# Kernel optimization log

Hardware: AMD Instinct MI355X
Metric: run time of the kernel (lower is better)

Reference implementation:

```python
import jax, jax.numpy as jnp
import numpy as np

N_TX, N_ACC, N_MER = 100000, 50000, 5000
HID, HEADS, OUT_CH, LAYERS = 128, 4, 64, 3
HC = HID * HEADS  # 512, concat-heads width
SRC_T = ['tx', 'tx', 'tx', 'acc', 'acc', 'mer']
DST_T = ['acc', 'acc', 'mer', 'tx', 'tx', 'tx']


def setup_inputs():
    key = jax.random.key(0)
    ks = jax.random.split(key, 16)
    rn = lambda k, s: jax.random.normal(k, s, dtype=jnp.float32) * 0.05
    n_of = {'tx': N_TX, 'acc': N_ACC, 'mer': N_MER}
    E = N_TX  # one sender-acct / receiver-acct / merchant edge per transaction
    src = jnp.stack([jax.random.randint(jax.random.fold_in(ks[0], r), (E,), 0, n_of[SRC_T[r]]) for r in range(6)])
    dst = jnp.stack([jax.random.randint(jax.random.fold_in(ks[1], r), (E,), 0, n_of[DST_T[r]]) for r in range(6)])
    edges = jnp.stack([src, dst], axis=1).astype(jnp.int32)  # [6, 2, E] (rel, src/dst, edge)
    return dict(
        x_tx=rn(ks[2], (N_TX, 64)), x_acc=rn(ks[3], (N_ACC, 32)), x_mer=rn(ks[4], (N_MER, 32)),
        Wtx=rn(ks[5], (64, HID)), btx=jnp.zeros((HID,), jnp.float32),
        Wacc=rn(ks[6], (32, HID)), bacc=jnp.zeros((HID,), jnp.float32),
        Wmer=rn(ks[7], (32, HID)), bmer=jnp.zeros((HID,), jnp.float32),
        W0=rn(ks[8], (6, HID, HC)),            # layer-0 GAT linear per relation
        Wrest=rn(ks[9], (LAYERS - 1, 6, HC, HC)),  # layers 1..L-1
        att_s=rn(ks[10], (LAYERS, 6, HEADS, HID)),
        att_d=rn(ks[11], (LAYERS, 6, HEADS, HID)),
        att_b=jnp.zeros((LAYERS, 6, HC), jnp.float32),
        bn_g=jnp.ones((LAYERS, HC), jnp.float32), bn_b=jnp.zeros((LAYERS, HC), jnp.float32),
        Wh1=rn(ks[12], (HC, OUT_CH)), bh1=jnp.zeros((OUT_CH,), jnp.float32),
        Wh2=rn(ks[13], (OUT_CH, 1)), bh2=jnp.zeros((1,), jnp.float32),
        edges=edges)


def _gat_rel(x_src, x_dst, src, dst, W, a_s, a_d, b, n_dst):
    """PyG GATConv (shared lin, add_self_loops=False, concat heads), eval mode."""
    H, C = a_s.shape
    hs = (x_src @ W).reshape(-1, H, C)  # [Ns, H, C]
    hd = (x_dst @ W).reshape(-1, H, C)  # [Nd, H, C]
    e = jax.nn.leaky_relu((hs * a_s).sum(-1)[src] + (hd * a_d).sum(-1)[dst], 0.2)  # [E, H]
    m = jax.lax.stop_gradient(jax.ops.segment_max(e, dst, num_segments=n_dst))
    ex = jnp.exp(e - m[dst])
    denom = jax.ops.segment_sum(ex, dst, num_segments=n_dst)
    alpha = ex / (denom[dst] + 1e-16)  # segment softmax over in-edges of each dst
    out = jax.ops.segment_sum(alpha[:, :, None] * hs[src], dst, num_segments=n_dst)
    return out.reshape(n_dst, H * C) + b


def _forward(x_tx, x_acc, x_mer, Wtx, btx, Wacc, bacc, Wmer, bmer, W0, Wrest,
             att_s, att_d, att_b, bn_g, bn_b, Wh1, bh1, Wh2, bh2, edges):
    h = {'tx': jax.nn.relu(x_tx @ Wtx + btx),
         'acc': jax.nn.relu(x_acc @ Wacc + bacc),
         'mer': jax.nn.relu(x_mer @ Wmer + bmer)}
    n_of = {'tx': x_tx.shape[0], 'acc': x_acc.shape[0], 'mer': x_mer.shape[0]}
    for i in range(LAYERS):
        Wl = W0 if i == 0 else Wrest[i - 1]
        new = {k: jnp.zeros((n_of[k], HC), x_tx.dtype) for k in n_of}  # HeteroConv aggr='sum'
        for r in range(6):
            o = _gat_rel(h[SRC_T[r]], h[DST_T[r]], edges[r, 0], edges[r, 1],
                         Wl[r], att_s[i, r], att_d[i, r], att_b[i, r], n_of[DST_T[r]])
            new[DST_T[r]] = new[DST_T[r]] + o
        t = new['tx']  # BatchNorm1d (batch statistics) on transaction nodes only
        mu = t.mean(0)
        var = t.var(0)
        new['tx'] = (t - mu) / jnp.sqrt(var + 1e-5) * bn_g[i] + bn_b[i]
        new = {k: jax.nn.relu(v) for k, v in new.items()}
        if i > 0:  # residual from second layer on
            new = {k: new[k] + h[k] for k in new}
        h = new
    hidden = jax.nn.relu(h['tx'] @ Wh1 + bh1)
    return (hidden @ Wh2 + bh2).squeeze(-1)  # [N_tx] logits


def reference(x_tx, x_acc, x_mer, Wtx, btx, Wacc, bacc, Wmer, bmer, W0, Wrest,
              att_s, att_d, att_b, bn_g, bn_b, Wh1, bh1, Wh2, bh2, edges):
    return _forward(x_tx, x_acc, x_mer, Wtx, btx, Wacc, bacc, Wmer, bmer, W0, Wrest,
                    att_s, att_d, att_b, bn_g, bn_b, Wh1, bh1, Wh2, bh2, edges)
```

## Files before the change

### kernel.cpp

```cpp
#include <hip/hip_runtime.h>
#include <math.h>


typedef unsigned short BF16;
typedef short short8 __attribute__((ext_vector_type(8)));
typedef float f32x4 __attribute__((ext_vector_type(4)));
typedef __bf16 bf16x8 __attribute__((ext_vector_type(8)));

static __device__ __forceinline__ float lrelu(float x){ return x > 0.f ? x : 0.2f*x; }

__device__ __forceinline__ float ldE(const float* p, long i){ return p[i]; }
__device__ __forceinline__ float ldE(const BF16* p, long i){
  return __uint_as_float((unsigned)p[i] << 16);
}
__device__ __forceinline__ void stE(float* p, long i, float v){ p[i] = v; }
__device__ __forceinline__ void stE(BF16* p, long i, float v){
  unsigned u = __float_as_uint(v);
  p[i] = (BF16)((u + 0x7FFFu + ((u >> 16) & 1u)) >> 16);
}
__device__ __forceinline__ BF16 f2bf(float v){
  unsigned u = __float_as_uint(v);
  return (BF16)((u + 0x7FFFu + ((u >> 16) & 1u)) >> 16);
}
__device__ __forceinline__ float bf2f(short s){
  return __uint_as_float((unsigned)(unsigned short)s << 16);
}
__device__ __forceinline__ float4 ld4E(const float* p, long i){ return *(const float4*)(p + i); }
__device__ __forceinline__ float4 ld4E(const BF16* p, long i){
  ushort4 s = *(const ushort4*)(p + i);
  return make_float4(__uint_as_float((unsigned)s.x<<16), __uint_as_float((unsigned)s.y<<16),
                     __uint_as_float((unsigned)s.z<<16), __uint_as_float((unsigned)s.w<<16));
}

__global__ void k_zero(int* __restrict__ p, long n){
  long i = (long)blockIdx.x*blockDim.x + threadIdx.x;
  if (i < n) p[i] = 0;
}
__global__ void k_fill_f32(float* __restrict__ p, long n, float v){
  long i = (long)blockIdx.x*blockDim.x + threadIdx.x;
  if (i < n) p[i] = v;
}

__global__ __launch_bounds__(256) void k_wt(const float* __restrict__ in, BF16* __restrict__ out,
                                            int K, int N)
{
  __shared__ float t[32][33];
  int kb = blockIdx.y*32, nb = blockIdx.x*32;
  int tx = threadIdx.x & 31, ty8 = threadIdx.x >> 5;
  for (int j = ty8; j < 32; j += 8){
    int k = kb + j, n = nb + tx;
    t[j][tx] = (k < K && n < N) ? in[(long)k*N + n] : 0.f;
  }
  __syncthreads();
  for (int j = ty8; j < 32; j += 8){
    int n = nb + j, k = kb + tx;
    if (n < N && k < K) out[(long)n*K + k] = f2bf(t[tx][j]);
  }
}

__global__ __launch_bounds__(256) void k_foldAll(
    const float* __restrict__ Wbase, long wstride,
    const float* __restrict__ atts, const float* __restrict__ attd,
    float* __restrict__ F, int Din)
{
  int w = (blockIdx.x*256 + threadIdx.x) >> 6;
  int lane = threadIdx.x & 63;
  int total = 48*Din;
  if (w >= total) return;
  int k = w % Din;
  int rem = w / Din;
  int h = rem & 3, sd = (rem >> 2) & 1, r = rem >> 3;
  const float* wr = Wbase + (long)r*wstride + (long)k*512 + h*128;
  const float* ar = (sd ? attd : atts) + r*512 + h*128;
  float p = wr[lane]*ar[lane] + wr[lane+64]*ar[lane+64];
  #pragma unroll
  for (int off = 32; off; off >>= 1) p += __shfl_down(p, off, 64);
  if (lane == 0) F[(long)((r*2+sd)*4 + h)*Din + k] = p;
}

template<int BN, int WM, int WN, int FM, int FN, typename TC>
__global__ __launch_bounds__(256) void k_mfma(
    const BF16* __restrict__ A, const BF16* __restrict__ Bt, TC* __restrict__ C,
    int M, int K, int c0, int ldc, const float* __restrict__ bias, int doRelu)
{
  constexpr int BM = 128;
  constexpr int LSTR = 72;
  __shared__ __attribute__((aligned(16))) short Als[BM][LSTR];
  __shared__ __attribute__((aligned(16))) short Bls[BN][LSTR];
  const int bn0 = blockIdx.x * BN;
  const int bm = blockIdx.y*BM;
  const int tid = threadIdx.x;
  const int wave = tid >> 6, lane = tid & 63;
  const int wr = wave / WN, wc = wave % WN;
  const int lrow = lane & 15, kg = lane >> 4;
  f32x4 acc[FM][FN] = {};
  for (int k0 = 0; k0 < K; k0 += 64){
    #pragma unroll
    for (int t = 0; t < 4; ++t){
      int idx = tid + t*256;
      int row = idx >> 3, kc = (idx & 7) << 3;
      int gr = bm + row;
      short8 v = {};
      if (gr < M) v = *(const short8*)(A + (long)gr*K + k0 + kc);
      *(short8*)&Als[row][kc] = v;
    }
    #pragma unroll
    for (int t = 0; t < BN/32; ++t){
      int idx = tid + t*256;
      int row = idx >> 3, kc = (idx & 7) << 3;
      *(short8*)&Bls[row][kc] = *(const short8*)(Bt + (long)(c0+bn0+row)*K + k0 + kc);
    }
    __syncthreads();
    #pragma unroll
    for (int kk = 0; kk < 2; ++kk){
      short8 af[FM], bq[FN];
      #pragma unroll
      for (int m = 0; m < FM; ++m)
        af[m] = *(const short8*)&Als[wr*FM*16 + m*16 + lrow][kk*32 + kg*8];
      #pragma unroll
      for (int n = 0; n < FN; ++n)
        bq[n] = *(const short8*)&Bls[wc*FN*16 + n*16 + lrow][kk*32 + kg*8];
      #pragma unroll
      for (int m = 0; m < FM; ++m)
        #pragma unroll
        for (int n = 0; n < FN; ++n)
          acc[m][n] = __builtin_amdgcn_mfma_f32_16x16x32_bf16(
              __builtin_bit_cast(bf16x8, af[m]), __builtin_bit_cast(bf16x8, bq[n]),
              acc[m][n], 0, 0, 0);
    }
    __syncthreads();
  }
  #pragma unroll
  for (int m = 0; m < FM; ++m){
    #pragma unroll
    for (int n = 0; n < FN; ++n){
      #pragma unroll
      for (int j = 0; j < 4; ++j){
        int row = bm + wr*FM*16 + m*16 + kg*4 + j;
        if (row >= M) continue;
        int col = wc*FN*16 + n*16 + lrow;
        float v = acc[m][n][j];
        if (bias) v += bias[bn0 + col];
        if (doRelu) v = fmaxf(v, 0.f);
        stE(C, (long)row*ldc + bn0 + col, v);
      }
    }
  }
}

template<typename TA, typename TC>
__global__ __launch_bounds__(256) void k_gemm(
    const TA* __restrict__ A, const float* __restrict__ B, TC* __restrict__ C,
    int M, int N, int K, int ldb, const float* __restrict__ bias, int doRelu)
{
  __shared__ float As[16][64];
  __shared__ float Bs[16][64];
  const int bm = blockIdx.y*64, bn = blockIdx.x*64;
  const int tid = threadIdx.x;
  const int ty = tid >> 4, tx = tid & 15;
  const int ar = tid >> 2;
  const int ac = (tid & 3) << 2;
  const int br = tid >> 4;
  const int bc = (tid & 15) << 2;
  float acc[4][4] = {};
  for (int k0 = 0; k0 < K; k0 += 16){
    int row = bm + ar;
    float4 av = make_float4(0.f,0.f,0.f,0.f);
    if (row < M) av = ld4E(A, (long)row*K + k0 + ac);
    As[ac+0][ar]=av.x; As[ac+1][ar]=av.y; As[ac+2][ar]=av.z; As[ac+3][ar]=av.w;
    float4 bv = make_float4(0.f,0.f,0.f,0.f);
    if (bn + bc + 3 < N) bv = *(const float4*)(B + (long)(k0+br)*ldb + bn + bc);
    *(float4*)&Bs[br][bc] = bv;
    __syncthreads();
    #pragma unroll
    for (int kk = 0; kk < 16; ++kk){
      float a[4], b[4];
      #pragma unroll
      for (int x = 0; x < 4; ++x){ a[x]=As[kk][ty*4+x]; b[x]=Bs[kk][tx*4+x]; }
      #pragma unroll
      for (int y = 0; y < 4; ++y)
        #pragma unroll
        for (int x = 0; x < 4; ++x) acc[y][x] += a[y]*b[x];
    }
    __syncthreads();
  }
  #pragma unroll
  for (int y = 0; y < 4; ++y){
    int row = bm + ty*4 + y;
    if (row >= M) continue;
    #pragma unroll
    for (int x = 0; x < 4; ++x){
      int col = bn + tx*4 + x;
      if (col >= N) continue;
      float v = acc[y][x];
      if (bias) v += bias[col];
      if (doRelu) v = fmaxf(v, 0.f);
      stE(C, (long)row*N + col, v);
    }
  }
}

template<int R>
__global__ __launch_bounds__(256) void k_scoreM(
    const BF16* __restrict__ X, const float* __restrict__ Ftab, long fstride,
    float* __restrict__ out, long ostride, int N, int Din)
{
  int wave = threadIdx.x >> 6, lane = threadIdx.x & 63;
  int node0 = blockIdx.x*16 + wave*4;
  if (node0 >= N) return;
  int base = lane*8;
  bool act = base < Din;
  float x[4][8];
  #pragma unroll
  for (int t = 0; t < 4; ++t){
    int node = node0 + t;
    if (act && node < N){
      short8 v = *(const short8*)(X + (long)node*Din + base);
      #pragma unroll
      for (int j = 0; j < 8; ++j) x[t][j] = bf2f(v[j]);
    } else {
      #pragma unroll
      for (int j = 0; j < 8; ++j) x[t][j] = 0.f;
    }
  }
  #pragma unroll
  for (int r = 0; r < R; ++r){
    const float* F = Ftab + (long)r*fstride;
    float p[4][4] = {};
    #pragma unroll
    for (int h = 0; h < 4; ++h){
      float f[8];
      if (act){
        float4 fa = *(const float4*)(F + h*Din + base);
        float4 fb = *(const float4*)(F + h*Din + base + 4);
        f[0]=fa.x; f[1]=fa.y; f[2]=fa.z; f[3]=fa.w;
        f[4]=fb.x; f[5]=fb.y; f[6]=fb.z; f[7]=fb.w;
      } else {
        #pragma unroll
        for (int j = 0; j < 8; ++j) f[j] = 0.f;
      }
      #pragma unroll
      for (int t = 0; t < 4; ++t)
        #pragma unroll
        for (int j = 0; j < 8; ++j) p[t][h] += x[t][j]*f[j];
    }
    #pragma unroll
    for (int t = 0; t < 4; ++t)
      #pragma unroll
      for (int h = 0; h < 4; ++h)
        #pragma unroll
        for (int off = 32; off; off >>= 1)
          p[t][h] += __shfl_down(p[t][h], off, 64);
    if (lane == 0){
      #pragma unroll
      for (int t = 0; t < 4; ++t){
        int node = node0 + t;
        if (node < N){
          #pragma unroll
          for (int h = 0; h < 4; ++h)
            out[(long)r*ostride + (long)node*4 + h] = p[t][h];
        }
      }
    }
  }
}

__global__ void k_hist(const int* __restrict__ dst, int* __restrict__ counts, int E, int nd){
  int e = blockIdx.x*blockDim.x + threadIdx.x;
  if (e >= E) return;
  int d = dst[e];
  if ((unsigned)d < (unsigned)nd) atomicAdd(&counts[d], 1);
}
__global__ void k_scan1(const int* __restrict__ counts, int* __restrict__ indptr,
                        int* __restrict__ bsums, int n)
{
  __shared__ int sm[256];
  int i = blockIdx.x*256 + threadIdx.x;
  int v = (i < n) ? counts[i] : 0;
  sm[threadIdx.x] = v; __syncthreads();
  for (int off = 1; off < 256; off <<= 1){
    int t = (threadIdx.x >= off) ? sm[threadIdx.x - off] : 0;
    __syncthreads();
    sm[threadIdx.x] += t;
    __syncthreads();
  }
  if (i < n) indptr[i+1] = sm[threadIdx.x];
  if (threadIdx.x == 255) bsums[blockIdx.x] = sm[255];
  if (blockIdx.x == 0 && threadIdx.x == 0) indptr[0] = 0;
}
__global__ void k_scan2(int* __restrict__ bsums, int nb){
  __shared__ int sm[1024];
  int t = threadIdx.x;
  int v = (t < nb) ? bsums[t] : 0;
  sm[t] = v; __syncthreads();
  for (int off = 1; off < 1024; off <<= 1){
    int x = (t >= off) ? sm[t - off] : 0;
    __syncthreads();
    sm[t] += x;
    __syncthreads();
  }
  if (t < nb) bsums[t] = sm[t];
}
__global__ void k_scan3(int* __restrict__ indptr, const int* __restrict__ bsums, int n){
  if (blockIdx.x == 0) return;
  int i = blockIdx.x*256 + threadIdx.x;
  int add = bsums[blockIdx.x - 1];
  if (i < n) indptr[i+1] += add;
}
__global__ void k_scatter(const int* __restrict__ src, const int* __restrict__ dst,
                          const int* __restrict__ indptr, int* __restrict__ cursor,
                          int* __restrict__ esrc, int E, int nd, int ns)
{
  int e = blockIdx.x*blockDim.x + threadIdx.x;
  if (e >= E) return;
  int d = dst[e];
  if ((unsigned)d >= (unsigned)nd) return;
  int s = src[e];
  if ((unsigned)s >= (unsigned)ns) s = 0;
  int pos = indptr[d] + atomicAdd(&cursor[d], 1);
  if (pos >= 0 && pos < E) esrc[pos] = s;
}

__global__ __launch_bounds__(256) void k_alpha(
    const float* __restrict__ ss, const float* __restrict__ sd,
    const int* __restrict__ indptr, const int* __restrict__ esrc,
    float* __restrict__ alpha, int n_dst, int E, int ns)
{
  int wid = (blockIdx.x*blockDim.x + threadIdx.x) >> 6;
  int lane = threadIdx.x & 63;
  if (wid >= n_dst) return;
  int e0 = indptr[wid], e1 = indptr[wid+1];
  e0 = max(0, min(e0, E)); e1 = max(e0, min(e1, E));
  if (e0 >= e1) return;
  int h = lane >> 4, g = lane & 15;
  float sdl = sd[(long)wid*4 + h];
  float m = -INFINITY;
  for (int e = e0 + g; e < e1; e += 16){
    int s = esrc[e]; if ((unsigned)s >= (unsigned)ns) s = 0;
    m = fmaxf(m, lrelu(ss[(long)s*4 + h] + sdl));
  }
  #pragma unroll
  for (int o = 1; o < 16; o <<= 1) m = fmaxf(m, __shfl_xor(m, o, 16));
  float den = 0.f;
  for (int e = e0 + g; e < e1; e += 16){
    int s = esrc[e]; if ((unsigned)s >= (unsigned)ns) s = 0;
    den += __expf(lrelu(ss[(long)s*4 + h] + sdl) - m);
  }
  #pragma unroll
  for (int o = 1; o < 16; o <<= 1) den += __shfl_xor(den, o, 16);
  float inv = 1.f/(den + 1e-16f);
  for (int e = e0 + g; e < e1; e += 16){
    int s = esrc[e]; if ((unsigned)s >= (unsigned)ns) s = 0;
    alpha[(long)e*4 + h] = __expf(lrelu(ss[(long)s*4 + h] + sdl) - m) * inv;
  }
}

__device__ __forceinline__ void agg_body(
    const BF16* __restrict__ Zt, const float* __restrict__ alpha,
    const int* __restrict__ indptr, const int* __restrict__ esrc,
    float* acc, int NJ, int wid, int lane, int TW, int head0, int E, int ns)
{
  int e0 = indptr[wid], e1 = indptr[wid+1];
  e0 = max(0, min(e0, E)); e1 = max(e0, min(e1, E));
  for (int e = e0; e < e1; ++e){
    int s = esrc[e]; if ((unsigned)s >= (unsigned)ns) s = 0;
    float aA = alpha[(long)e*4 + head0];
    float aB = (NJ == 4) ? alpha[(long)e*4 + head0 + 1] : aA;
    const BF16* zr = Zt + (long)s*TW;
    #pragma unroll 4
    for (int j = 0; j < NJ; ++j){
      int col = lane + 64*j;
      if (col < TW) acc[j] += ((NJ == 4 && j >= 2) ? aB : aA) * ldE(zr, col);
    }
  }
}
template<int NJ>
__global__ __launch_bounds__(256) void k_agg(
    const BF16* __restrict__ Zt, const float* __restrict__ alpha,
    const int* __restrict__ indptr, const int* __restrict__ esrc,
    BF16* __restrict__ out, int ldc, int c0w, int TW, int head0,
    int accum, int n_dst, int E, int ns)
{
  int wid = (blockIdx.x*blockDim.x + threadIdx.x) >> 6;
  int lane = threadIdx.x & 63;
  if (wid >= n_dst) return;
  float acc[NJ];
  #pragma unroll
  for (int j = 0; j < NJ; ++j) acc[j] = 0.f;
  agg_body(Zt, alpha, indptr, esrc, acc, NJ, wid, lane, TW, head0, E, ns);
  #pragma unroll
  for (int j = 0; j < NJ; ++j){
    int col = lane + 64*j;
    if (col < TW){
      long idx = (long)wid*ldc + c0w + col;
      float v = acc[j];
      if (accum) v += ldE(out, idx);
      stE(out, idx, v);
    }
  }
}

template<int NJ>
__global__ __launch_bounds__(256) void k_agg3(
    const BF16* __restrict__ Z0, const BF16* __restrict__ Z1, const BF16* __restrict__ Z2,
    const float* __restrict__ a0, const float* __restrict__ a1, const float* __restrict__ a2,
    const int* __restrict__ ip0, const int* __restrict__ ip1, const int* __restrict__ ip2,
    const int* __restrict__ es0, const int* __restrict__ es1, const int* __restrict__ es2,
    BF16* __restrict__ out, int ldc, int TW, int head0,
    int n_dst, int E, int ns0, int ns1, int ns2)
{
  int wid = (blockIdx.x*blockDim.x + threadIdx.x) >> 6;
  int lane = threadIdx.x & 63;
  if (wid >= n_dst) return;
  float acc[NJ];
  #pragma unroll
  for (int j = 0; j < NJ; ++j) acc[j] = 0.f;
  agg_body(Z0, a0, ip0, es0, acc, NJ, wid, lane, TW, head0, E, ns0);
  agg_body(Z1, a1, ip1, es1, acc, NJ, wid, lane, TW, head0, E, ns1);
  agg_body(Z2, a2, ip2, es2, acc, NJ, wid, lane, TW, head0, E, ns2);
  #pragma unroll
  for (int j = 0; j < NJ; ++j){
    int col = lane + 64*j;
    if (col < TW) stE(out, (long)wid*ldc + col, acc[j]);
  }
}

__global__ void k_bnp(const BF16* __restrict__ nw, float* __restrict__ bnp,
                      int N, int TW, int P)
{
  int col  = threadIdx.x & (TW - 1);
  int slot = threadIdx.x / TW;
  int rpb  = 256 / TW;
  int p    = blockIdx.x*rpb + slot;
  float s = 0.f, s2 = 0.f;
  for (long r = p; r < N; r += P){
    float v = ldE(nw, r*TW + col);
    s += v; s2 += v*v;
  }
  bnp[(long)p*2*TW + col]      = s;
  bnp[(long)p*2*TW + TW + col] = s2;
}
__global__ void k_bnf(const float* __restrict__ bnp, float* __restrict__ bns,
                      int P, int TW)
{
  int c = blockIdx.x*256 + threadIdx.x;
  if (c >= 2*TW) return;
  float s = 0.f;
  for (int p = 0; p < P; ++p) s += bnp[(long)p*2*TW + c];
  bns[c] = s;
}
__global__ void k_bn_apply(const BF16* __restrict__ nw, const float* __restrict__ bns,
                           const float* __restrict__ g, const float* __restrict__ b,
                           BF16* __restrict__ A, int N, int TW, int c0, int res)
{
  long total = (long)N*TW;
  for (long i = (long)blockIdx.x*blockDim.x + threadIdx.x; i < total;
       i += (long)gridDim.x*blockDim.x){
    int col = (int)(i % TW);
    long r  = i / TW;
    float mu  = bns[col] / (float)N;
    float var = bns[TW + col] / (float)N - mu*mu;
    int gc = c0 + col;
    float sc = g[gc] * rsqrtf(var + 1e-5f);
    float sh = b[gc] - mu*sc;
    float v = fmaxf(ldE(nw, i)*sc + sh, 0.f);
    long ai = r*512 + gc;
    if (res) v += ldE(A, ai);
    stE(A, ai, v);
  }
}

__global__ void k_update(const BF16* __restrict__ B, const float* __restrict__ ab1,
                         const float* __restrict__ ab2, BF16* __restrict__ A,
                         long n512, int res)
{
  for (long i = (long)blockIdx.x*blockDim.x + threadIdx.x; i < n512;
       i += (long)gridDim.x*blockDim.x){
    int c = (int)(i & 511);
    float v = ldE(B, i) + ab1[c] + (ab2 ? ab2[c] : 0.f);
    v = fmaxf(v, 0.f);
    if (res) v += ldE(A, i);
    stE(A, i, v);
  }
}

__global__ void k_logits(const BF16* __restrict__ Hid, const float* __restrict__ Wh2,
                         const float* __restrict__ bh2, float* __restrict__ out, int N)
{
  int node = (blockIdx.x*blockDim.x + threadIdx.x) >> 6;
  int lane = threadIdx.x & 63;
  if (node >= N) return;
  float v = ldE(Hid, (long)node*64 + lane) * Wh2[lane];
  #pragma unroll
  for (int off = 32; off; off >>= 1) v += __shfl_down(v, off, 64);
  if (lane == 0) out[node] = v + bh2[0];
}

struct Arena {
  BF16 *A[3];
  BF16 *Bst[3];
  BF16 *Zt;
  BF16 *nwtile;
  BF16 *hidden;
  float *scoreS, *scoreD;
  float *alpha;
  float *Fbuf;
  float *bnp, *bns;
  int *counts, *bsums;
  int *indptr[6], *esrc[6];
  BF16 *Wt0[6], *WtL[2][6], *Wh1t;
  size_t total;
};

extern "C" void kernel_launch(void* const* d_in, const int* in_sizes, int n_in,
                              void* d_out, int out_size, void* d_ws, size_t ws_size,
                              hipStream_t stream)
{
  const float* x_tx  = (const float*)d_in[0];
  const float* x_acc = (const float*)d_in[1];
  const float* x_mer = (const float*)d_in[2];
  const float* Wtx = (const float*)d_in[3];  const float* btx  = (const float*)d_in[4];
  const float* Wacc= (const float*)d_in[5];  const float* bacc = (const float*)d_in[6];
  const float* Wmer= (const float*)d_in[7];  const float* bmer = (const float*)d_in[8];
  const float* W0   = (const float*)d_in[9];
  const float* Wrest= (const float*)d_in[10];
  const float* att_s= (const float*)d_in[11];
  const float* att_d= (const float*)d_in[12];
  const float* att_b= (const float*)d_in[13];
  const float* bn_g = (const float*)d_in[14];
  const float* bn_b = (const float*)d_in[15];
  const float* Wh1  = (const float*)d_in[16]; const float* bh1 = (const float*)d_in[17];
  const float* Wh2  = (const float*)d_in[18]; const float* bh2 = (const float*)d_in[19];
  const int*   edges= (const int*)d_in[20];

  const int E    = in_sizes[20] / 12;
  const int nTx  = in_sizes[0] / 64;
  const int nAcc = in_sizes[1] / 32;
  const int nMer = in_sizes[2] / 32;
  const int nOf[3]   = {nTx, nAcc, nMer};
  const int SRC_T[6] = {0,0,0,1,1,2};
  const int DST_T[6] = {1,1,2,0,0,0};
  const int maxN = max(nTx, max(nAcc, nMer));
  (void)n_in;

  auto layout = [&](int TW)->Arena{
    Arena P{};
    size_t off = 0;
    auto a = [&](size_t bytes)->char*{
      char* p = (char*)d_ws + off;
      off += (bytes + 255) & ~(size_t)255;
      return p;
    };
    auto al = [](size_t b){ return (b + 255) & ~(size_t)255; };
    P.A[0]   = (BF16*)a((size_t)nTx *512*2);
    P.A[1]   = (BF16*)a((size_t)nAcc*512*2);
    P.A[2]   = (BF16*)a((size_t)nMer*512*2);
    P.Bst[1] = (BF16*)a((size_t)nAcc*512*2);
    P.Bst[2] = (BF16*)a((size_t)nMer*512*2);
    size_t zrows = (size_t)maxN > (size_t)2*nAcc + nMer ? (size_t)maxN : (size_t)2*nAcc + nMer;
    size_t zB  = al(zrows*TW*2);
    size_t nwB = al((size_t)nTx*TW*2);
    size_t scoreB = al((size_t)3*maxN*4*4)*2;
    size_t hidB= al((size_t)nTx*64*2);
    size_t scr = zB + nwB;
    if (scr < scoreB) scr = scoreB;
    if (scr < hidB)   scr = hidB;
    char* scrBase = a(scr);
    P.Zt     = (BF16*)scrBase;
    P.nwtile = (BF16*)(scrBase + zB);
    P.scoreS = (float*)scrBase;
    P.scoreD = (float*)(scrBase + al((size_t)3*maxN*4*4));
    P.hidden = (BF16*)scrBase;
    P.alpha  = (float*)a((size_t)3*E*4*4);
    P.Fbuf   = (float*)a((size_t)6*8*512*4);
    P.bnp    = (float*)a(262144);
    P.bns    = (float*)a(4096);
    P.counts = (int*)a((size_t)maxN*4);
    P.bsums  = (int*)a(4096);
    for (int r = 0; r < 6; ++r){
      P.indptr[r] = (int*)a((size_t)(nOf[DST_T[r]]+1)*4);
      P.esrc[r]   = (int*)a((size_t)E*4);
    }
    for (int r = 0; r < 6; ++r) P.Wt0[r] = (BF16*)a((size_t)512*128*2);
    for (int l = 0; l < 2; ++l)
      for (int r = 0; r < 6; ++r) P.WtL[l][r] = (BF16*)a((size_t)512*512*2);
    P.Wh1t = (BF16*)a((size_t)64*512*2);
    P.total = off;
    return P;
  };

  int TW = 0;
  Arena P{};
  for (int cand : {256, 128, 64}){
    P = layout(cand);
    if (P.total <= ws_size){ TW = cand; break; }
  }
  if (TW == 0){
    float sentinel = 10000.0f + (float)(ws_size >> 20);
    k_fill_f32<<<dim3((out_size+255)/256), dim3(256), 0, stream>>>((float*)d_out, (long)out_size, sentinel);
    return;
  }
  const int nTiles = 512 / TW;
  const int NJv = TW/64;
  const int rpb = 256 / TW, PBX = 128, Pp = PBX * rpb;
  dim3 b256(256);

  for (int r = 0; r < 6; ++r)
    k_wt<<<dim3(16,4), b256, 0, stream>>>(W0 + (size_t)r*128*512, P.Wt0[r], 128, 512);
  for (int l = 0; l < 2; ++l)
    for (int r = 0; r < 6; ++r)
      k_wt<<<dim3(16,16), b256, 0, stream>>>(Wrest + ((size_t)l*6 + r)*512*512, P.WtL[l][r], 512, 512);
  k_wt<<<dim3(2,16), b256, 0, stream>>>(Wh1, P.Wh1t, 512, 64);

  auto mfma_gemm = [&](const BF16* A, const BF16* Bt, BF16* Cp, int M, int K, int c0, int ldc){
    if (TW >= 128)
      k_mfma<128,2,2,4,4,BF16><<<dim3(TW/128,(M+127)/128),b256,0,stream>>>(A, Bt, Cp, M, K, c0, ldc, (const float*)nullptr, 0);
    else
      k_mfma<64,4,1,2,4,BF16><<<dim3(1,(M+127)/128),b256,0,stream>>>(A, Bt, Cp, M, K, c0, ldc, (const float*)nullptr, 0);
  };
  auto agg1 = [&](const BF16* Zt, const float* al, const int* ip, const int* es,
                  BF16* out, int ldc, int c0w, int head0, int accum, int nd, int ns){
    dim3 g((nd+3)/4);
    if (NJv == 4)      k_agg<4><<<g,b256,0,stream>>>(Zt, al, ip, es, out, ldc, c0w, TW, head0, accum, nd, E, ns);
    else if (NJv == 2) k_agg<2><<<g,b256,0,stream>>>(Zt, al, ip, es, out, ldc, c0w, TW, head0, accum, nd, E, ns);
    else               k_agg<1><<<g,b256,0,stream>>>(Zt, al, ip, es, out, ldc, c0w, TW, head0, accum, nd, E, ns);
  };

  for (int r = 0; r < 6; ++r){
    int nd = nOf[DST_T[r]], ns = nOf[SRC_T[r]];
    const int* srcP = edges + (size_t)r*2*E;
    const int* dstP = srcP + E;
    int nb = (nd + 255)/256;
    k_zero   <<<dim3(nb),          b256, 0, stream>>>(P.counts, (long)nd);
    k_hist   <<<dim3((E+255)/256), b256, 0, stream>>>(dstP, P.counts, E, nd);
    k_scan1  <<<dim3(nb),          b256, 0, stream>>>(P.counts, P.indptr[r], P.bsums, nd);
    k_scan2  <<<dim3(1),           dim3(1024),0, stream>>>(P.bsums, nb);
    k_scan3  <<<dim3(nb),          b256, 0, stream>>>(P.indptr[r], P.bsums, nd);
    k_zero   <<<dim3(nb),          b256, 0, stream>>>(P.counts, (long)nd);
    k_scatter<<<dim3((E+255)/256), b256, 0, stream>>>(srcP, dstP, P.indptr[r], P.counts, P.esrc[r], E, nd, ns);
  }

  k_gemm<float,BF16><<<dim3(2,(nTx +63)/64), b256, 0, stream>>>(x_tx,  Wtx,  P.A[0], nTx,  128, 64, 128, btx,  1);
  k_gemm<float,BF16><<<dim3(2,(nAcc+63)/64), b256, 0, stream>>>(x_acc, Wacc, P.A[1], nAcc, 128, 32, 128, bacc, 1);
  k_gemm<float,BF16><<<dim3(2,(nMer+63)/64), b256, 0, stream>>>(x_mer, Wmer, P.A[2], nMer, 128, 32, 128, bmer, 1);

  const long mS = (long)maxN*4;
  for (int i = 0; i < 3; ++i){
    const int Din = (i == 0) ? 128 : 512;
    const int res = (i > 0) ? 1 : 0;
    const long fstr = 8L*Din;
    const float* WbaseL = (i == 0) ? W0 : (Wrest + (size_t)(i-1)*6*512*512);
    const long wstride = (i == 0) ? 128L*512 : 512L*512;
    auto Wtof = [&](int r)->const BF16*{ return (i == 0) ? P.Wt0[r] : P.WtL[i-1][r]; };

    k_foldAll<<<dim3(48*Din/4), b256, 0, stream>>>(WbaseL, wstride,
        att_s + (size_t)i*6*512, att_d + (size_t)i*6*512, P.Fbuf, Din);

    k_scoreM<3><<<dim3((nTx+15)/16), b256, 0, stream>>>(P.A[0], P.Fbuf,           fstr, P.scoreS, mS, nTx, Din);
    k_scoreM<2><<<dim3((nAcc+15)/16), b256, 0, stream>>>(P.A[1], P.Fbuf + 4*Din,  fstr, P.scoreD, mS, nAcc, Din);
    k_scoreM<1><<<dim3((nMer+15)/16), b256, 0, stream>>>(P.A[2], P.Fbuf + 20*Din, fstr, P.scoreD + 2*mS, 0, nMer, Din);
    for (int r = 0; r < 3; ++r){
      int nd = nOf[DST_T[r]];
      k_alpha<<<dim3((nd+3)/4), b256, 0, stream>>>(P.scoreS + r*mS, P.scoreD + r*mS,
          P.indptr[r], P.esrc[r], P.alpha + (size_t)r*E*4, nd, E, nTx);
    }
    for (int r = 0; r < 3; ++r){
      int dt = DST_T[r], nd = nOf[dt];
      int accF = (r == 1) ? 1 : 0;
      for (int t = 0; t < nTiles; ++t){
        int c0 = t*TW;
        mfma_gemm(P.A[0], Wtof(r), P.Zt, nTx, Din, c0, TW);
        agg1(P.Zt, P.alpha + (size_t)r*E*4, P.indptr[r], P.esrc[r],
             P.Bst[dt], 512, c0, c0 >> 7, accF, nd, nTx);
      }
    }

    k_scoreM<2><<<dim3((nAcc+15)/16), b256, 0, stream>>>(P.A[1], P.Fbuf + 24*Din, fstr, P.scoreS, mS, nAcc, Din);
    k_scoreM<1><<<dim3((nMer+15)/16), b256, 0, stream>>>(P.A[2], P.Fbuf + 40*Din, fstr, P.scoreS + 2*mS, 0, nMer, Din);
    k_scoreM<3><<<dim3((nTx+15)/16), b256, 0, stream>>>(P.A[0], P.Fbuf + 28*Din, fstr, P.scoreD, mS, nTx, Din);
    for (int q = 0; q < 3; ++q){
      int r = 3 + q;
      k_alpha<<<dim3((nTx+3)/4), b256, 0, stream>>>(P.scoreS + q*mS, P.scoreD + q*mS,
          P.indptr[r], P.esrc[r], P.alpha + (size_t)q*E*4, nTx, E, nOf[SRC_T[r]]);
    }
    BF16* Z3 = P.Zt;
    BF16* Z4 = P.Zt + (size_t)nAcc*TW;
    BF16* Z5 = P.Zt + (size_t)2*nAcc*TW;
    for (int t = 0; t < nTiles; ++t){
      int c0 = t*TW;
      mfma_gemm(P.A[1], Wtof(3), Z3, nAcc, Din, c0, TW);
      mfma_gemm(P.A[1], Wtof(4), Z4, nAcc, Din, c0, TW);
      mfma_gemm(P.A[2], Wtof(5), Z5, nMer, Din, c0, TW);
      dim3 ga((nTx+3)/4);
      if (NJv == 4)
        k_agg3<4><<<ga,b256,0,stream>>>(Z3,Z4,Z5, P.alpha, P.alpha+(size_t)E*4, P.alpha+(size_t)2*E*4,
            P.indptr[3],P.indptr[4],P.indptr[5], P.esrc[3],P.esrc[4],P.esrc[5],
            P.nwtile, TW, TW, c0>>7, nTx, E, nAcc, nAcc, nMer);
      else if (NJv == 2)
        k_agg3<2><<<ga,b256,0,stream>>>(Z3,Z4,Z5, P.alpha, P.alpha+(size_t)E*4, P.alpha+(size_t)2*E*4,
            P.indptr[3],P.indptr[4],P.indptr[5], P.esrc[3],P.esrc[4],P.esrc[5],
            P.nwtile, TW, TW, c0>>7, nTx, E, nAcc, nAcc, nMer);
      else
        k_agg3<1><<<ga,b256,0,stream>>>(Z3,Z4,Z5, P.alpha, P.alpha+(size_t)E*4, P.alpha+(size_t)2*E*4,
            P.indptr[3],P.indptr[4],P.indptr[5], P.esrc[3],P.esrc[4],P.esrc[5],
            P.nwtile, TW, TW, c0>>7, nTx, E, nAcc, nAcc, nMer);
      k_bnp<<<dim3(PBX), b256, 0, stream>>>(P.nwtile, P.bnp, nTx, TW, Pp);
      k_bnf<<<dim3((2*TW+255)/256), b256, 0, stream>>>(P.bnp, P.bns, Pp, TW);
      k_bn_apply<<<dim3(2048), b256, 0, stream>>>(P.nwtile, P.bns,
          bn_g + (size_t)i*512, bn_b + (size_t)i*512, P.A[0], nTx, TW, c0, res);
    }
    const float* ab0 = att_b + ((size_t)(i*6 + 0))*512;
    const float* ab1 = att_b + ((size_t)(i*6 + 1))*512;
    const float* ab2 = att_b + ((size_t)(i*6 + 2))*512;
    k_update<<<dim3(2048), b256, 0, stream>>>(P.Bst[1], ab0, ab1, P.A[1], (long)nAcc*512, res);
    k_update<<<dim3(256),  b256, 0, stream>>>(P.Bst[2], ab2, (const float*)nullptr, P.A[2], (long)nMer*512, res);
  }

  k_mfma<64,4,1,2,4,BF16><<<dim3(1,(nTx+127)/128), b256, 0, stream>>>(
      P.A[0], P.Wh1t, P.hidden, nTx, 512, 0, 64, bh1, 1);
  k_logits<<<dim3((nTx+3)/4), b256, 0, stream>>>(P.hidden, Wh2, bh2, (float*)d_out, nTx);
}
```

Baseline: 11.54 ms.

## Aggregate-then-transform for merchant relation and fuse tx→acc relation aggregations

For the tx→merchant relation, source features are first gathered and weighted per head by alpha into a small per-merchant buffer, and only then multiplied by W. This avoids projecting all 100k transaction rows for a destination set of 5k nodes. The two tx→acc relations are now projected into separate buffers and aggregated in one k_agg2 launch, which removes the read-modify-write accumulate pass. The trade-off is a larger scratch layout, and tile width 256 is dropped as a candidate.

New measurement: 10.73 ms. -7.0%, faster.

```diff
diff --git a/kernel.cpp b/kernel.cpp
--- a/kernel.cpp
+++ b/kernel.cpp
@@ -81,7 +81,8 @@
 template<int BN, int WM, int WN, int FM, int FN, typename TC>
 __global__ __launch_bounds__(256) void k_mfma(
     const BF16* __restrict__ A, const BF16* __restrict__ Bt, TC* __restrict__ C,
-    int M, int K, int c0, int ldc, const float* __restrict__ bias, int doRelu)
+    int M, int K, int c0, int ldc, int lda, const float* __restrict__ bias,
+    int doRelu, int accum)
 {
   constexpr int BM = 128;
   constexpr int LSTR = 72;
@@ -101,7 +102,7 @@
       int row = idx >> 3, kc = (idx & 7) << 3;
       int gr = bm + row;
       short8 v = {};
-      if (gr < M) v = *(const short8*)(A + (long)gr*K + k0 + kc);
+      if (gr < M) v = *(const short8*)(A + (long)gr*lda + k0 + kc);
       *(short8*)&Als[row][kc] = v;
     }
     #pragma unroll
@@ -142,7 +143,9 @@
         float v = acc[m][n][j];
         if (bias) v += bias[bn0 + col];
         if (doRelu) v = fmaxf(v, 0.f);
-        stE(C, (long)row*ldc + bn0 + col, v);
+        long idx = (long)row*ldc + bn0 + col;
+        if (accum) v += ldE(C, idx);
+        stE(C, idx, v);
       }
     }
   }
@@ -355,6 +358,40 @@
   }
 }
 
+template<int NJ>
+__global__ __launch_bounds__(256) void k_gather4(
+    const BF16* __restrict__ A, const float* __restrict__ alpha,
+    const int* __restrict__ indptr, const int* __restrict__ esrc,
+    BF16* __restrict__ G, int n_dst, int Din, int E, int ns)
+{
+  int wid = (blockIdx.x*blockDim.x + threadIdx.x) >> 6;
+  int lane = threadIdx.x & 63;
+  if (wid >= n_dst) return;
+  int e0 = indptr[wid], e1 = indptr[wid+1];
+  e0 = max(0, min(e0, E)); e1 = max(e0, min(e1, E));
+  float acc[4][NJ];
+  #pragma unroll
+  for (int h = 0; h < 4; ++h)
+    #pragma unroll
+    for (int j = 0; j < NJ; ++j) acc[h][j] = 0.f;
+  for (int e = e0; e < e1; ++e){
+    int s = esrc[e]; if ((unsigned)s >= (unsigned)ns) s = 0;
+    float a0 = alpha[(long)e*4 + 0], a1 = alpha[(long)e*4 + 1];
+    float a2 = alpha[(long)e*4 + 2], a3 = alpha[(long)e*4 + 3];
+    const BF16* ar = A + (long)s*Din;
+    #pragma unroll
+    for (int j = 0; j < NJ; ++j){
+      float x = ldE(ar, lane + 64*j);
+      acc[0][j] += a0*x; acc[1][j] += a1*x; acc[2][j] += a2*x; acc[3][j] += a3*x;
+    }
+  }
+  #pragma unroll
+  for (int h = 0; h < 4; ++h)
+    #pragma unroll
+    for (int j = 0; j < NJ; ++j)
+      stE(G, ((long)wid*4 + h)*Din + lane + 64*j, acc[h][j]);
+}
+
 __device__ __forceinline__ void agg_body(
     const BF16* __restrict__ Zt, const float* __restrict__ alpha,
     const int* __restrict__ indptr, const int* __restrict__ esrc,
@@ -374,12 +411,15 @@
     }
   }
 }
+
 template<int NJ>
-__global__ __launch_bounds__(256) void k_agg(
-    const BF16* __restrict__ Zt, const float* __restrict__ alpha,
-    const int* __restrict__ indptr, const int* __restrict__ esrc,
+__global__ __launch_bounds__(256) void k_agg2(
+    const BF16* __restrict__ Z0, const BF16* __restrict__ Z1,
+    const float* __restrict__ a0, const float* __restrict__ a1,
+    const int* __restrict__ ip0, const int* __restrict__ ip1,
+    const int* __restrict__ es0, const int* __restrict__ es1,
     BF16* __restrict__ out, int ldc, int c0w, int TW, int head0,
-    int accum, int n_dst, int E, int ns)
+    int n_dst, int E, int ns0, int ns1)
 {
   int wid = (blockIdx.x*blockDim.x + threadIdx.x) >> 6;
   int lane = threadIdx.x & 63;
@@ -387,16 +427,12 @@
   float acc[NJ];
   #pragma unroll
   for (int j = 0; j < NJ; ++j) acc[j] = 0.f;
-  agg_body(Zt, alpha, indptr, esrc, acc, NJ, wid, lane, TW, head0, E, ns);
+  agg_body(Z0, a0, ip0, es0, acc, NJ, wid, lane, TW, head0, E, ns0);
+  agg_body(Z1, a1, ip1, es1, acc, NJ, wid, lane, TW, head0, E, ns1);
   #pragma unroll
   for (int j = 0; j < NJ; ++j){
     int col = lane + 64*j;
-    if (col < TW){
-      long idx = (long)wid*ldc + c0w + col;
-      float v = acc[j];
-      if (accum) v += ldE(out, idx);
-      stE(out, idx, v);
-    }
+    if (col < TW) stE(out, (long)wid*ldc + c0w + col, acc[j]);
   }
 }
 
@@ -500,7 +536,7 @@
   BF16 *A[3];
   BF16 *Bst[3];
   BF16 *Zt;
-  BF16 *nwtile;
+  BF16 *blkB;
   BF16 *hidden;
   float *scoreS, *scoreD;
   float *alpha;
@@ -557,17 +593,19 @@
     P.A[2]   = (BF16*)a((size_t)nMer*512*2);
     P.Bst[1] = (BF16*)a((size_t)nAcc*512*2);
     P.Bst[2] = (BF16*)a((size_t)nMer*512*2);
-    size_t zrows = (size_t)maxN > (size_t)2*nAcc + nMer ? (size_t)maxN : (size_t)2*nAcc + nMer;
-    size_t zB  = al(zrows*TW*2);
-    size_t nwB = al((size_t)nTx*TW*2);
+    size_t zrowsA = (size_t)maxN > (size_t)2*nAcc + nMer ? (size_t)maxN : (size_t)2*nAcc + nMer;
+    size_t blkA = al(zrowsA*TW*2);
+    size_t blkBsz = al((size_t)nTx*TW*2);
+    size_t gB = al((size_t)nMer*4*512*2);
+    if (gB > blkBsz) blkBsz = gB;
     size_t scoreB = al((size_t)3*maxN*4*4)*2;
-    size_t hidB= al((size_t)nTx*64*2);
-    size_t scr = zB + nwB;
+    size_t hidB = al((size_t)nTx*64*2);
+    size_t scr = blkA + blkBsz;
     if (scr < scoreB) scr = scoreB;
     if (scr < hidB)   scr = hidB;
     char* scrBase = a(scr);
     P.Zt     = (BF16*)scrBase;
-    P.nwtile = (BF16*)(scrBase + zB);
+    P.blkB   = (BF16*)(scrBase + blkA);
     P.scoreS = (float*)scrBase;
     P.scoreD = (float*)(scrBase + al((size_t)3*maxN*4*4));
     P.hidden = (BF16*)scrBase;
@@ -591,7 +629,7 @@
 
   int TW = 0;
   Arena P{};
-  for (int cand : {256, 128, 64}){
+  for (int cand : {128, 64}){
     P = layout(cand);
     if (P.total <= ws_size){ TW = cand; break; }
   }
@@ -614,16 +652,9 @@
 
   auto mfma_gemm = [&](const BF16* A, const BF16* Bt, BF16* Cp, int M, int K, int c0, int ldc){
     if (TW >= 128)
-      k_mfma<128,2,2,4,4,BF16><<<dim3(TW/128,(M+127)/128),b256,0,stream>>>(A, Bt, Cp, M, K, c0, ldc, (const float*)nullptr, 0);
+      k_mfma<128,2,2,4,4,BF16><<<dim3(TW/128,(M+127)/128),b256,0,stream>>>(A, Bt, Cp, M, K, c0, ldc, K, (const float*)nullptr, 0, 0);
     else
-      k_mfma<64,4,1,2,4,BF16><<<dim3(1,(M+127)/128),b256,0,stream>>>(A, Bt, Cp, M, K, c0, ldc, (const float*)nullptr, 0);
-  };
-  auto agg1 = [&](const BF16* Zt, const float* al, const int* ip, const int* es,
-                  BF16* out, int ldc, int c0w, int head0, int accum, int nd, int ns){
-    dim3 g((nd+3)/4);
-    if (NJv == 4)      k_agg<4><<<g,b256,0,stream>>>(Zt, al, ip, es, out, ldc, c0w, TW, head0, accum, nd, E, ns);
-    else if (NJv == 2) k_agg<2><<<g,b256,0,stream>>>(Zt, al, ip, es, out, ldc, c0w, TW, head0, accum, nd, E, ns);
-    else               k_agg<1><<<g,b256,0,stream>>>(Zt, al, ip, es, out, ldc, c0w, TW, head0, accum, nd, E, ns);
+      k_mfma<64,4,1,2,4,BF16><<<dim3(1,(M+127)/128),b256,0,stream>>>(A, Bt, Cp, M, K, c0, ldc, K, (const float*)nullptr, 0, 0);
   };
 
   for (int r = 0; r < 6; ++r){
@@ -664,14 +695,35 @@
       k_alpha<<<dim3((nd+3)/4), b256, 0, stream>>>(P.scoreS + r*mS, P.scoreD + r*mS,
           P.indptr[r], P.esrc[r], P.alpha + (size_t)r*E*4, nd, E, nTx);
     }
-    for (int r = 0; r < 3; ++r){
-      int dt = DST_T[r], nd = nOf[dt];
-      int accF = (r == 1) ? 1 : 0;
+    {
+      BF16* Gm = P.blkB;
+      if (Din == 512)
+        k_gather4<8><<<dim3((nMer+3)/4), b256, 0, stream>>>(P.A[0], P.alpha + (size_t)2*E*4,
+            P.indptr[2], P.esrc[2], Gm, nMer, Din, E, nTx);
+      else
+        k_gather4<2><<<dim3((nMer+3)/4), b256, 0, stream>>>(P.A[0], P.alpha + (size_t)2*E*4,
+            P.indptr[2], P.esrc[2], Gm, nMer, Din, E, nTx);
+      for (int h = 0; h < 4; ++h)
+        k_mfma<128,2,2,4,4,BF16><<<dim3(1,(nMer+127)/128), b256, 0, stream>>>(
+            Gm + (size_t)h*Din, Wtof(2), P.Bst[2] + (size_t)h*128,
+            nMer, Din, h*128, 512, 4*Din, (const float*)nullptr, 0, 0);
+    }
+    {
+      BF16* Zr0 = P.Zt;
+      BF16* Zr1 = P.blkB;
       for (int t = 0; t < nTiles; ++t){
         int c0 = t*TW;
-        mfma_gemm(P.A[0], Wtof(r), P.Zt, nTx, Din, c0, TW);
-        agg1(P.Zt, P.alpha + (size_t)r*E*4, P.indptr[r], P.esrc[r],
-             P.Bst[dt], 512, c0, c0 >> 7, accF, nd, nTx);
+        mfma_gemm(P.A[0], Wtof(0), Zr0, nTx, Din, c0, TW);
+        mfma_gemm(P.A[0], Wtof(1), Zr1, nTx, Din, c0, TW);
+        dim3 ga((nAcc+3)/4);
+        if (NJv == 2)
+          k_agg2<2><<<ga,b256,0,stream>>>(Zr0, Zr1, P.alpha, P.alpha + (size_t)E*4,
+              P.indptr[0], P.indptr[1], P.esrc[0], P.esrc[1],
+              P.Bst[1], 512, c0, TW, c0>>7, nAcc, E, nTx, nTx);
+        else
+          k_agg2<1><<<ga,b256,0,stream>>>(Zr0, Zr1, P.alpha, P.alpha + (size_t)E*4,
+              P.indptr[0], P.indptr[1], P.esrc[0], P.esrc[1],
+              P.Bst[1], 512, c0, TW, c0>>7, nAcc, E, nTx, nTx);
       }
     }
 
@@ -686,27 +738,24 @@
     BF16* Z3 = P.Zt;
     BF16* Z4 = P.Zt + (size_t)nAcc*TW;
     BF16* Z5 = P.Zt + (size_t)2*nAcc*TW;
+    BF16* nw = P.blkB;
     for (int t = 0; t < nTiles; ++t){
       int c0 = t*TW;
       mfma_gemm(P.A[1], Wtof(3), Z3, nAcc, Din, c0, TW);
       mfma_gemm(P.A[1], Wtof(4), Z4, nAcc, Din, c0, TW);
       mfma_gemm(P.A[2], Wtof(5), Z5, nMer, Din, c0, TW);
       dim3 ga((nTx+3)/4);
-      if (NJv == 4)
-        k_agg3<4><<<ga,b256,0,stream>>>(Z3,Z4,Z5, P.alpha, P.alpha+(size_t)E*4, P.alpha+(size_t)2*E*4,
-            P.indptr[3],P.indptr[4],P.indptr[5], P.esrc[3],P.esrc[4],P.esrc[5],
-            P.nwtile, TW, TW, c0>>7, nTx, E, nAcc, nAcc, nMer);
-      else if (NJv == 2)
+      if (NJv == 2)
         k_agg3<2><<<ga,b256,0,stream>>>(Z3,Z4,Z5, P.alpha, P.alpha+(size_t)E*4, P.alpha+(size_t)2*E*4,
             P.indptr[3],P.indptr[4],P.indptr[5], P.esrc[3],P.esrc[4],P.esrc[5],
-            P.nwtile, TW, TW, c0>>7, nTx, E, nAcc, nAcc, nMer);
+            nw, TW, TW, c0>>7, nTx, E, nAcc, nAcc, nMer);
       else
         k_agg3<1><<<ga,b256,0,stream>>>(Z3,Z4,Z5, P.alpha, P.alpha+(size_t)E*4, P.alpha+(size_t)2*E*4,
             P.indptr[3],P.indptr[4],P.indptr[5], P.esrc[3],P.esrc[4],P.esrc[5],
-            P.nwtile, TW, TW, c0>>7, nTx, E, nAcc, nAcc, nMer);
-      k_bnp<<<dim3(PBX), b256, 0, stream>>>(P.nwtile, P.bnp, nTx, TW, Pp);
+            nw, TW, TW, c0>>7, nTx, E, nAcc, nAcc, nMer);
+      k_bnp<<<dim3(PBX), b256, 0, stream>>>(nw, P.bnp, nTx, TW, Pp);
       k_bnf<<<dim3((2*TW+255)/256), b256, 0, stream>>>(P.bnp, P.bns, Pp, TW);
-      k_bn_apply<<<dim3(2048), b256, 0, stream>>>(P.nwtile, P.bns,
+      k_bn_apply<<<dim3(2048), b256, 0, stream>>>(nw, P.bns,
           bn_g + (size_t)i*512, bn_b + (size_t)i*512, P.A[0], nTx, TW, c0, res);
     }
     const float* ab0 = att_b + ((size_t)(i*6 + 0))*512;
@@ -717,6 +766,6 @@
   }
 
   k_mfma<64,4,1,2,4,BF16><<<dim3(1,(nTx+127)/128), b256, 0, stream>>>(
-      P.A[0], P.Wh1t, P.hidden, nTx, 512, 0, 64, bh1, 1);
+      P.A[0], P.Wh1t, P.hidden, nTx, 512, 0, 64, 512, bh1, 1, 0);
   k_logits<<<dim3((nTx+3)/4), b256, 0, stream>>>(P.hidden, Wh2, bh2, (float*)d_out, nTx);
 }
```
